# Performance work log

Measured on AMD Instinct MI355X. Metric: run time of the kernel, lower is better.

The kernel has to match this reference:

```python
import jax, jax.numpy as jnp
import numpy as np

B, PAD_LEN, HID, NB, NY = 1024, 127, 512, 128, 8
IN_DIM = 5 * (PAD_LEN + 1)          # LSTMCell input_size = 5*(pad_len+1)
MAX_TRIP, MAX_ROW = 10, 8
BARGE_PAR_WIDTH = 10.0


def setup_inputs() -> dict:
    key = jax.random.key(0)
    ks = jax.random.split(key, 12)
    s = 1.0 / np.sqrt(HID).astype(np.float32)
    return {
        "x": jax.random.normal(ks[0], (B, IN_DIM), jnp.float32),
        "h0": jnp.zeros((B, HID), jnp.float32),
        "c0": jnp.zeros((B, HID), jnp.float32),
        "W_ih": jax.random.normal(ks[1], (4 * HID, IN_DIM), jnp.float32) * s,
        "W_hh": jax.random.normal(ks[2], (4 * HID, HID), jnp.float32) * s,
        "b_ih": jax.random.normal(ks[3], (4 * HID,), jnp.float32) * s,
        "b_hh": jax.random.normal(ks[4], (4 * HID,), jnp.float32) * s,
        "W_fc": jax.random.normal(ks[5], (NB * NY, HID), jnp.float32) * s,
        "b_fc": jax.random.normal(ks[6], (NB * NY,), jnp.float32) * s,
        "block_size": jax.random.uniform(ks[7], (B, NB, 5), jnp.float32),
        "block_lengths_on_barge": jax.random.uniform(ks[8], (B, NY, MAX_TRIP, MAX_ROW), jnp.float32),
        "block_width_on_barge": jax.random.uniform(ks[9], (B, NY, MAX_TRIP, MAX_ROW), jnp.float32),
        "encoder_mask": jax.random.bernoulli(ks[10], 0.5, (B, NB, NY, PAD_LEN)),
        "block_mask": jnp.zeros((B, NB), bool),
        "barge_count": jax.random.randint(ks[11], (B, NY), 0, MAX_TRIP, jnp.int32),
        "barge_slot": -jnp.ones((B, NY, MAX_TRIP, MAX_ROW, 2), jnp.int32),
    }


def reference(x, h0, c0, W_ih, W_hh, b_ih, b_hh, W_fc, b_fc,
              block_size, block_lengths_on_barge, block_width_on_barge,
              encoder_mask, block_mask, barge_count, barge_slot):
    # ---- LSTMCell step (torch gate order: i, f, g, o) ----
    gates = x @ W_ih.T + b_ih + h0 @ W_hh.T + b_hh          # (B, 4H)
    i, f, g, o = jnp.split(gates, 4, axis=-1)
    c = jax.nn.sigmoid(f) * c0 + jax.nn.sigmoid(i) * jnp.tanh(g)
    h = jax.nn.sigmoid(o) * jnp.tanh(c)

    # ---- fc + masked softmax over (block, yard) joint actions ----
    logits = h @ W_fc.T + b_fc                               # (B, NB*NY)
    yard_feasible = jnp.any(encoder_mask, axis=-1)           # (B, NB, NY): block fits in some slot of yard
    valid = yard_feasible & (~block_mask)[:, :, None]        # unselected blocks only
    neg = jnp.asarray(-1e9, logits.dtype)
    probs = jax.nn.softmax(jnp.where(valid.reshape(valid.shape[0], -1), logits, neg), axis=-1)

    # ---- action decode + per-sample barge-slot scatter allocation ----
    Bsz = x.shape[0]
    bidx = jnp.arange(Bsz)
    action = jnp.argmax(probs, axis=-1)                      # greedy selection
    block_sel = action // NY
    yard_sel = (action % NY).astype(barge_count.dtype)
    cur = barge_count[bidx, yard_sel]                        # (B,) current barge idx per sample
    blen = block_size[bidx, block_sel, 0]                    # (B,)
    bwid = block_size[bidx, block_sel, 1]                    # (B,)

    widths = block_width_on_barge[bidx, yard_sel, cur]       # (B, MAX_ROW) gathered rows
    lens = block_lengths_on_barge[bidx, yard_sel, cur]       # (B, MAX_ROW)
    par_ok = widths <= BARGE_PAR_WIDTH                       # parallel-space feasibility per slot
    cand = jnp.where(par_ok, lens, -1.0)                     # invalid slots -> -1 (as in source)
    slot = jnp.argmax(cand, axis=-1)                         # best existing-length parallel slot

    barge_slot_new = barge_slot.at[bidx, yard_sel, cur, slot, 1].set(block_sel.astype(barge_slot.dtype))
    widths_new = block_width_on_barge.at[bidx, yard_sel, cur, slot].add(bwid)
    lengths_new = block_lengths_on_barge.at[bidx, yard_sel, cur, slot].max(blen)
    return probs, barge_slot_new, lengths_new, widths_new
```

## Files before the change

### kernel.cpp

```cpp
#include <hip/hip_runtime.h>
#include <math.h>

#define Bsz 1024
#define PADL 127
#define HID 512
#define NBb 128
#define NYd 8
#define INDIM 640
#define MTRIP 10
#define MROW 8
#define NBNY 1024
#define FOURH 2048

__device__ __forceinline__ float sigf(float x){ return 1.0f/(1.0f+expf(-x)); }

template<int TM>
__global__ __launch_bounds__(256) void gemm_bias(
    const float* __restrict__ A1, const float* __restrict__ B1, int K1,
    const float* __restrict__ A2, const float* __restrict__ B2, int K2,
    const float* __restrict__ bias1, const float* __restrict__ bias2,
    float* __restrict__ C, int ldc)
{
    constexpr int BM = TM*16;
    __shared__ float As[2][16][BM+4];
    __shared__ float Bs[2][16][68];
    const int tid = threadIdx.x;
    const int m0 = blockIdx.y*BM, n0 = blockIdx.x*64;

    const int ar = (TM==8) ? (tid>>1) : (tid>>2);
    const int ac = (TM==8) ? ((tid&1)*8) : ((tid&3)*4);
    const int br = tid>>2, bc = (tid&3)*4;

    const int tm = (tid>>4)*TM, tn = (tid&15)*4;

    float acc[TM][4];
    #pragma unroll
    for (int i=0;i<TM;i++){
        #pragma unroll
        for (int j=0;j<4;j++) acc[i][j]=0.f;
    }

    const int P1 = K1/16;
    const int nsteps = P1 + K2/16;

    float4 pa0, pa1, pb0;
    auto prefetch = [&](int s){
        const float* A; const float* B; int K; int k0;
        if (s < P1){ A=A1; B=B1; K=K1; k0 = s*16; }
        else       { A=A2; B=B2; K=K2; k0 = (s-P1)*16; }
        const float* ap = A + (size_t)(m0+ar)*K + k0 + ac;
        pa0 = *(const float4*)ap;
        if (TM==8) pa1 = *(const float4*)(ap+4);
        pb0 = *(const float4*)(B + (size_t)(n0+br)*K + k0 + bc);
    };
    auto stage = [&](int buf){
        As[buf][ac+0][ar]=pa0.x; As[buf][ac+1][ar]=pa0.y;
        As[buf][ac+2][ar]=pa0.z; As[buf][ac+3][ar]=pa0.w;
        if (TM==8){
            As[buf][ac+4][ar]=pa1.x; As[buf][ac+5][ar]=pa1.y;
            As[buf][ac+6][ar]=pa1.z; As[buf][ac+7][ar]=pa1.w;
        }
        Bs[buf][bc+0][br]=pb0.x; Bs[buf][bc+1][br]=pb0.y;
        Bs[buf][bc+2][br]=pb0.z; Bs[buf][bc+3][br]=pb0.w;
    };

    prefetch(0);
    stage(0);
    __syncthreads();
    int buf = 0;
    for (int s=0; s<nsteps; ++s){
        if (s+1 < nsteps) prefetch(s+1);
        #pragma unroll
        for (int kk=0; kk<16; ++kk){
            float a[TM], b[4];
            #pragma unroll
            for (int i=0;i<TM;i++) a[i] = As[buf][kk][tm+i];
            #pragma unroll
            for (int j=0;j<4;j++)  b[j] = Bs[buf][kk][tn+j];
            #pragma unroll
            for (int i=0;i<TM;i++)
                #pragma unroll
                for (int j=0;j<4;j++) acc[i][j] += a[i]*b[j];
        }
        if (s+1 < nsteps){
            stage(buf^1);
            __syncthreads();
            buf ^= 1;
        }
    }

    #pragma unroll
    for (int i=0;i<TM;i++){
        int row = m0+tm+i;
        #pragma unroll
        for (int j=0;j<4;j++){
            int col = n0+tn+j;
            float bsum = bias1[col] + (bias2 ? bias2[col] : 0.f);
            C[(size_t)row*ldc + col] = acc[i][j] + bsum;
        }
    }
}

__global__ __launch_bounds__(256) void lstm_kernel(const float* __restrict__ gates,
    const float* __restrict__ c0, float* __restrict__ h)
{
    int idx = blockIdx.x*256 + threadIdx.x;
    int b = idx >> 7, j4 = (idx & 127)*4;
    const float* g = gates + (size_t)b*FOURH;
    float4 iv = *(const float4*)(g + j4);
    float4 fv = *(const float4*)(g + 512 + j4);
    float4 gv = *(const float4*)(g + 1024 + j4);
    float4 ov = *(const float4*)(g + 1536 + j4);
    float4 cv = *(const float4*)(c0 + (size_t)b*HID + j4);
    float4 hv;
    hv.x = sigf(ov.x)*tanhf(sigf(fv.x)*cv.x + sigf(iv.x)*tanhf(gv.x));
    hv.y = sigf(ov.y)*tanhf(sigf(fv.y)*cv.y + sigf(iv.y)*tanhf(gv.y));
    hv.z = sigf(ov.z)*tanhf(sigf(fv.z)*cv.z + sigf(iv.z)*tanhf(gv.z));
    hv.w = sigf(ov.w)*tanhf(sigf(fv.w)*cv.w + sigf(iv.w)*tanhf(gv.w));
    *(float4*)(h + (size_t)b*HID + j4) = hv;
}

__device__ __forceinline__ int row_any(const int* __restrict__ p){
    #pragma unroll 1
    for (int j=0; j<124; j+=4){
        if (p[j] | p[j+1] | p[j+2] | p[j+3]) return 1;
    }
    return (p[124] | p[125] | p[126]) ? 1 : 0;
}

__global__ __launch_bounds__(256) void softmax_fused(
    const float* __restrict__ logits, const int* __restrict__ em,
    const int* __restrict__ bmask, const int* __restrict__ bcount,
    const float* __restrict__ bsize, const float* __restrict__ bwid_in,
    const float* __restrict__ blen_in,
    float* __restrict__ probs,
    int* __restrict__ pslot, int* __restrict__ pblock,
    float* __restrict__ pblen, float* __restrict__ pbwid)
{
    int b = blockIdx.x, t = threadIdx.x;
    __shared__ float red[256];
    __shared__ int  redi[256];
    const float* lrow = logits + (size_t)b*NBNY;

    float ml[4]; float mymax = -INFINITY;
    #pragma unroll
    for (int r=0;r<4;++r){
        int c = t + r*256;
        int nb = c >> 3;
        int v = 0;
        if (bmask[b*NBb + nb] == 0)
            v = row_any(em + (size_t)(b*NBNY + c)*PADL);
        float m = v ? lrow[c] : -1e9f;
        ml[r] = m; mymax = fmaxf(mymax, m);
    }
    red[t]=mymax; __syncthreads();
    for (int s=128;s>0;s>>=1){ if(t<s) red[t]=fmaxf(red[t],red[t+s]); __syncthreads(); }
    float rowmax = red[0]; __syncthreads();

    float p[4]; float mysum=0.f;
    #pragma unroll
    for (int r=0;r<4;++r){ p[r]=expf(ml[r]-rowmax); mysum+=p[r]; }
    red[t]=mysum; __syncthreads();
    for (int s=128;s>0;s>>=1){ if(t<s) red[t]+=red[t+s]; __syncthreads(); }
    float inv = 1.0f/red[0]; __syncthreads();

    float bv=-INFINITY; int bi=0;
    #pragma unroll
    for (int r=0;r<4;++r){
        int c = t + r*256;
        float pr = p[r]*inv;
        probs[(size_t)b*NBNY + c] = pr;
        if (pr > bv){ bv=pr; bi=c; }
    }
    red[t]=bv; redi[t]=bi; __syncthreads();
    for (int s=128;s>0;s>>=1){
        if (t<s){
            float ov=red[t+s]; int oi=redi[t+s];
            if (ov>red[t] || (ov==red[t] && oi<redi[t])){ red[t]=ov; redi[t]=oi; }
        }
        __syncthreads();
    }

    if (t==0){
        int a = redi[0];
        int blk = a / NYd, yard = a % NYd;
        int cur = bcount[b*NYd + yard];
        int base = ((b*NYd + yard)*MTRIP + cur)*MROW;
        float bestv = -INFINITY; int bests = 0;
        #pragma unroll
        for (int s=0;s<MROW;++s){
            float w = bwid_in[base+s];
            float l = blen_in[base+s];
            float cand = (w <= 10.0f) ? l : -1.0f;
            if (cand > bestv){ bestv=cand; bests=s; }
        }
        pslot[b]  = base + bests;
        pblock[b] = blk;
        pblen[b]  = bsize[(b*NBb + blk)*5 + 0];
        pbwid[b]  = bsize[(b*NBb + blk)*5 + 1];
    }
}

__global__ __launch_bounds__(256) void finalize_kernel(const int* __restrict__ bslot,
    const float* __restrict__ blen_in, const float* __restrict__ bwid_in,
    const int* __restrict__ pslot, const int* __restrict__ pblock,
    const float* __restrict__ pblen, const float* __restrict__ pbwid,
    float* __restrict__ out_slot, float* __restrict__ out_len, float* __restrict__ out_wid)
{
    int i = blockIdx.x*256 + threadIdx.x;
    if (i < Bsz*NYd*MTRIP*MROW*2){
        int b = i / (NYd*MTRIP*MROW*2);
        float v = (float)bslot[i];
        if (i == pslot[b]*2 + 1) v = (float)pblock[b];
        out_slot[i] = v;
    }
    if (i < Bsz*NYd*MTRIP*MROW){
        int b = i / (NYd*MTRIP*MROW);
        float l = blen_in[i], w = bwid_in[i];
        if (i == pslot[b]){ l = fmaxf(l, pblen[b]); w = w + pbwid[b]; }
        out_len[i] = l;
        out_wid[i] = w;
    }
}

extern "C" void kernel_launch(void* const* d_in, const int* in_sizes, int n_in,
                              void* d_out, int out_size, void* d_ws, size_t ws_size,
                              hipStream_t stream)
{
    const float* x    = (const float*)d_in[0];
    const float* h0   = (const float*)d_in[1];
    const float* c0   = (const float*)d_in[2];
    const float* Wih  = (const float*)d_in[3];
    const float* Whh  = (const float*)d_in[4];
    const float* bih  = (const float*)d_in[5];
    const float* bhh  = (const float*)d_in[6];
    const float* Wfc  = (const float*)d_in[7];
    const float* bfc  = (const float*)d_in[8];
    const float* bsize= (const float*)d_in[9];
    const float* blen = (const float*)d_in[10];
    const float* bwid = (const float*)d_in[11];
    const int*   em   = (const int*)d_in[12];
    const int*   bmask= (const int*)d_in[13];
    const int*   bcount=(const int*)d_in[14];
    const int*   bslot= (const int*)d_in[15];

    float* out      = (float*)d_out;
    float* probs    = out;
    float* out_slot = out + 1048576;
    float* out_len  = out + 1048576 + 1310720;
    float* out_wid  = out_len + 655360;

    float* ws     = (float*)d_ws;
    float* gates  = ws;
    float* h      = ws + 2097152;
    float* logits = ws + 2621440;
    int*   pslot  = (int*)(ws + 3670016);
    int*   pblock = (int*)(ws + 3671040);
    float* pblen  = ws + 3672064;
    float* pbwid  = ws + 3673088;

    gemm_bias<8><<<dim3(FOURH/64, Bsz/128), 256, 0, stream>>>(
        x, Wih, INDIM, h0, Whh, HID, bih, bhh, gates, FOURH);
    lstm_kernel<<<512, 256, 0, stream>>>(gates, c0, h);
    gemm_bias<4><<<dim3(NBNY/64, Bsz/64), 256, 0, stream>>>(
        h, Wfc, HID, nullptr, nullptr, 0, bfc, nullptr, logits, NBNY);
    softmax_fused<<<Bsz, 256, 0, stream>>>(logits, em, bmask, bcount, bsize, bwid, blen,
                                           probs, pslot, pblock, pblen, pbwid);
    finalize_kernel<<<5120, 256, 0, stream>>>(bslot, blen, bwid, pslot, pblock, pblen, pbwid,
                                              out_slot, out_len, out_wid);
}
```

Before: 810.0 us.

## Run gates GEMM on bf16x3 split-precision MFMA with concatenated K operands

Splits x|h0 and W_ih|W_hh into high and low bf16 parts, concatenated along K (1152), in two conversion kernels. The gates GEMM then runs on 16x16x32 bf16 MFMA using three products (hh, hl, lh) to approximate fp32 accuracy. The fc GEMM becomes a dedicated fp32 kernel with vectorized LDS reads. This trades scalar FP32 FMA work for matrix-core throughput, at the cost of extra conversion passes over the weights every call and a small precision loss.

```diff
diff --git a/kernel.cpp b/kernel.cpp
--- a/kernel.cpp
+++ b/kernel.cpp
@@ -11,92 +11,181 @@
 #define MROW 8
 #define NBNY 1024
 #define FOURH 2048
+#define KCAT 1152
+
+typedef short  bf16x8 __attribute__((ext_vector_type(8)));
+typedef float  f32x4  __attribute__((ext_vector_type(4)));
+typedef unsigned short u16x8 __attribute__((ext_vector_type(8)));
 
 __device__ __forceinline__ float sigf(float x){ return 1.0f/(1.0f+expf(-x)); }
 
-template<int TM>
-__global__ __launch_bounds__(256) void gemm_bias(
-    const float* __restrict__ A1, const float* __restrict__ B1, int K1,
-    const float* __restrict__ A2, const float* __restrict__ B2, int K2,
-    const float* __restrict__ bias1, const float* __restrict__ bias2,
-    float* __restrict__ C, int ldc)
-{
-    constexpr int BM = TM*16;
-    __shared__ float As[2][16][BM+4];
+__device__ __forceinline__ unsigned short bf16rn(float x){
+    unsigned int u = __float_as_uint(x);
+    unsigned int r = (u + 0x7FFFu + ((u>>16)&1u)) >> 16;
+    return (unsigned short)r;
+}
+
+__global__ __launch_bounds__(256) void convert_concat(
+    const float* __restrict__ src1, const float* __restrict__ src2,
+    unsigned short* __restrict__ dstH, unsigned short* __restrict__ dstL)
+{
+    int t = blockIdx.x*256 + threadIdx.x;
+    int r  = t / 144;
+    int c8 = t - r*144;
+    const float* p = (c8 < 80) ? (src1 + (size_t)r*INDIM + c8*8)
+                               : (src2 + (size_t)r*HID + (c8-80)*8);
+    float4 v0 = *(const float4*)p;
+    float4 v1 = *(const float4*)(p+4);
+    float v[8] = {v0.x,v0.y,v0.z,v0.w,v1.x,v1.y,v1.z,v1.w};
+    u16x8 hv, lv;
+    #pragma unroll
+    for (int i=0;i<8;++i){
+        unsigned short h = bf16rn(v[i]);
+        float hf = __uint_as_float(((unsigned int)h)<<16);
+        unsigned short l = bf16rn(v[i]-hf);
+        hv[i] = h; lv[i] = l;
+    }
+    size_t base = (size_t)r*KCAT + c8*8;
+    *(u16x8*)(dstH + base) = hv;
+    *(u16x8*)(dstL + base) = lv;
+}
+
+__global__ __launch_bounds__(256) void gemm_gates_mfma(
+    const unsigned short* __restrict__ Ah_g, const unsigned short* __restrict__ Al_g,
+    const unsigned short* __restrict__ Bh_g, const unsigned short* __restrict__ Bl_g,
+    const float* __restrict__ bih, const float* __restrict__ bhh,
+    float* __restrict__ gates)
+{
+    __shared__ __align__(16) unsigned short Ah_s[128*32];
+    __shared__ __align__(16) unsigned short Al_s[128*32];
+    __shared__ __align__(16) unsigned short Bh_s[64*32];
+    __shared__ __align__(16) unsigned short Bl_s[64*32];
+
+    const int t = threadIdx.x;
+    const int lane = t & 63;
+    const int w = t >> 6;
+    const int wr = w >> 1, wc = w & 1;
+    const int m0 = blockIdx.y*128, n0 = blockIdx.x*64;
+
+    const int fa0 = t*8;
+    const int fa1 = (256+t)*8;
+    const int fb  = t*8;
+    const int ar0 = fa0>>5, ac0 = fa0&31;
+    const int ar1 = fa1>>5, ac1 = fa1&31;
+    const int brow = fb>>5, bcol = fb&31;
+
+    f32x4 acc[4][2];
+    #pragma unroll
+    for (int m=0;m<4;++m){
+        #pragma unroll
+        for (int n=0;n<2;++n) acc[m][n] = (f32x4){0.f,0.f,0.f,0.f};
+    }
+
+    uint4 rah0, rah1, ral0, ral1, rbh, rbl;
+    auto load6 = [&](int k0){
+        rah0 = *(const uint4*)(Ah_g + (size_t)(m0+ar0)*KCAT + k0 + ac0);
+        rah1 = *(const uint4*)(Ah_g + (size_t)(m0+ar1)*KCAT + k0 + ac1);
+        ral0 = *(const uint4*)(Al_g + (size_t)(m0+ar0)*KCAT + k0 + ac0);
+        ral1 = *(const uint4*)(Al_g + (size_t)(m0+ar1)*KCAT + k0 + ac1);
+        rbh  = *(const uint4*)(Bh_g + (size_t)(n0+brow)*KCAT + k0 + bcol);
+        rbl  = *(const uint4*)(Bl_g + (size_t)(n0+brow)*KCAT + k0 + bcol);
+    };
+
+    load6(0);
+    for (int s=0; s<KCAT/32; ++s){
+        __syncthreads();
+        *(uint4*)&Ah_s[fa0] = rah0;  *(uint4*)&Ah_s[fa1] = rah1;
+        *(uint4*)&Al_s[fa0] = ral0;  *(uint4*)&Al_s[fa1] = ral1;
+        *(uint4*)&Bh_s[fb]  = rbh;   *(uint4*)&Bl_s[fb]  = rbl;
+        __syncthreads();
+        if (s+1 < KCAT/32) load6((s+1)*32);
+
+        const int kc = (lane>>4)*8;
+        bf16x8 afh[4], afl[4], bfh[2], bfl[2];
+        #pragma unroll
+        for (int m=0;m<4;++m){
+            int idx = (wr*64 + m*16 + (lane&15))*32 + kc;
+            afh[m] = *(const bf16x8*)&Ah_s[idx];
+            afl[m] = *(const bf16x8*)&Al_s[idx];
+        }
+        #pragma unroll
+        for (int n=0;n<2;++n){
+            int idx = (wc*32 + n*16 + (lane&15))*32 + kc;
+            bfh[n] = *(const bf16x8*)&Bh_s[idx];
+            bfl[n] = *(const bf16x8*)&Bl_s[idx];
+        }
+        #pragma unroll
+        for (int m=0;m<4;++m){
+            #pragma unroll
+            for (int n=0;n<2;++n){
+                acc[m][n] = __builtin_amdgcn_mfma_f32_16x16x32_bf16(afh[m], bfh[n], acc[m][n], 0,0,0);
+                acc[m][n] = __builtin_amdgcn_mfma_f32_16x16x32_bf16(afh[m], bfl[n], acc[m][n], 0,0,0);
+                acc[m][n] = __builtin_amdgcn_mfma_f32_16x16x32_bf16(afl[m], bfh[n], acc[m][n], 0,0,0);
+            }
+        }
+    }
+
+    #pragma unroll
+    for (int m=0;m<4;++m){
+        #pragma unroll
+        for (int n=0;n<2;++n){
+            int row = m0 + wr*64 + m*16 + ((lane>>4)<<2);
+            int col = n0 + wc*32 + n*16 + (lane&15);
+            float bsum = bih[col] + bhh[col];
+            #pragma unroll
+            for (int q=0;q<4;++q)
+                gates[(size_t)(row+q)*FOURH + col] = acc[m][n][q] + bsum;
+        }
+    }
+}
+
+__global__ __launch_bounds__(256) void gemm_fc_f32(
+    const float* __restrict__ A, const float* __restrict__ B,
+    const float* __restrict__ bias, float* __restrict__ C)
+{
+    __shared__ float As[2][16][68];
     __shared__ float Bs[2][16][68];
     const int tid = threadIdx.x;
-    const int m0 = blockIdx.y*BM, n0 = blockIdx.x*64;
-
-    const int ar = (TM==8) ? (tid>>1) : (tid>>2);
-    const int ac = (TM==8) ? ((tid&1)*8) : ((tid&3)*4);
-    const int br = tid>>2, bc = (tid&3)*4;
-
-    const int tm = (tid>>4)*TM, tn = (tid&15)*4;
-
-    float acc[TM][4];
-    #pragma unroll
-    for (int i=0;i<TM;i++){
-        #pragma unroll
-        for (int j=0;j<4;j++) acc[i][j]=0.f;
-    }
-
-    const int P1 = K1/16;
-    const int nsteps = P1 + K2/16;
-
-    float4 pa0, pa1, pb0;
-    auto prefetch = [&](int s){
-        const float* A; const float* B; int K; int k0;
-        if (s < P1){ A=A1; B=B1; K=K1; k0 = s*16; }
-        else       { A=A2; B=B2; K=K2; k0 = (s-P1)*16; }
-        const float* ap = A + (size_t)(m0+ar)*K + k0 + ac;
-        pa0 = *(const float4*)ap;
-        if (TM==8) pa1 = *(const float4*)(ap+4);
-        pb0 = *(const float4*)(B + (size_t)(n0+br)*K + k0 + bc);
+    const int m0 = blockIdx.y*64, n0 = blockIdx.x*64;
+    const int lr = tid>>2, lc = (tid&3)*4;
+    const int tm = (tid>>4)*4, tn = (tid&15)*4;
+    float acc[4][4] = {{0,0,0,0},{0,0,0,0},{0,0,0,0},{0,0,0,0}};
+
+    float4 pa, pb;
+    auto prefetch = [&](int k0){
+        pa = *(const float4*)(A + (size_t)(m0+lr)*HID + k0 + lc);
+        pb = *(const float4*)(B + (size_t)(n0+lr)*HID + k0 + lc);
     };
     auto stage = [&](int buf){
-        As[buf][ac+0][ar]=pa0.x; As[buf][ac+1][ar]=pa0.y;
-        As[buf][ac+2][ar]=pa0.z; As[buf][ac+3][ar]=pa0.w;
-        if (TM==8){
-            As[buf][ac+4][ar]=pa1.x; As[buf][ac+5][ar]=pa1.y;
-            As[buf][ac+6][ar]=pa1.z; As[buf][ac+7][ar]=pa1.w;
-        }
-        Bs[buf][bc+0][br]=pb0.x; Bs[buf][bc+1][br]=pb0.y;
-        Bs[buf][bc+2][br]=pb0.z; Bs[buf][bc+3][br]=pb0.w;
+        As[buf][lc+0][lr]=pa.x; As[buf][lc+1][lr]=pa.y;
+        As[buf][lc+2][lr]=pa.z; As[buf][lc+3][lr]=pa.w;
+        Bs[buf][lc+0][lr]=pb.x; Bs[buf][lc+1][lr]=pb.y;
+        Bs[buf][lc+2][lr]=pb.z; Bs[buf][lc+3][lr]=pb.w;
     };
 
-    prefetch(0);
-    stage(0);
-    __syncthreads();
+    prefetch(0); stage(0); __syncthreads();
     int buf = 0;
-    for (int s=0; s<nsteps; ++s){
-        if (s+1 < nsteps) prefetch(s+1);
+    for (int s=0; s<HID/16; ++s){
+        if (s+1 < HID/16) prefetch((s+1)*16);
         #pragma unroll
         for (int kk=0; kk<16; ++kk){
-            float a[TM], b[4];
+            float4 a = *(const float4*)&As[buf][kk][tm];
+            float4 b = *(const float4*)&Bs[buf][kk][tn];
+            float a4[4]={a.x,a.y,a.z,a.w}, b4[4]={b.x,b.y,b.z,b.w};
             #pragma unroll
-            for (int i=0;i<TM;i++) a[i] = As[buf][kk][tm+i];
-            #pragma unroll
-            for (int j=0;j<4;j++)  b[j] = Bs[buf][kk][tn+j];
-            #pragma unroll
-            for (int i=0;i<TM;i++)
+            for (int i=0;i<4;i++)
                 #pragma unroll
-                for (int j=0;j<4;j++) acc[i][j] += a[i]*b[j];
-        }
-        if (s+1 < nsteps){
-            stage(buf^1);
-            __syncthreads();
-            buf ^= 1;
-        }
-    }
-
-    #pragma unroll
-    for (int i=0;i<TM;i++){
+                for (int j=0;j<4;j++) acc[i][j] += a4[i]*b4[j];
+        }
+        if (s+1 < HID/16){ stage(buf^1); __syncthreads(); buf ^= 1; }
+    }
+    #pragma unroll
+    for (int i=0;i<4;i++){
         int row = m0+tm+i;
         #pragma unroll
         for (int j=0;j<4;j++){
             int col = n0+tn+j;
-            float bsum = bias1[col] + (bias2 ? bias2[col] : 0.f);
-            C[(size_t)row*ldc + col] = acc[i][j] + bsum;
+            C[(size_t)row*NBNY + col] = acc[i][j] + bias[col];
         }
     }
 }
@@ -254,16 +343,21 @@
     float* gates  = ws;
     float* h      = ws + 2097152;
     float* logits = ws + 2621440;
-    int*   pslot  = (int*)(ws + 3670016);
-    int*   pblock = (int*)(ws + 3671040);
-    float* pblen  = ws + 3672064;
-    float* pbwid  = ws + 3673088;
-
-    gemm_bias<8><<<dim3(FOURH/64, Bsz/128), 256, 0, stream>>>(
-        x, Wih, INDIM, h0, Whh, HID, bih, bhh, gates, FOURH);
+    unsigned short* Ah = (unsigned short*)(ws + 3670016);
+    unsigned short* Al = (unsigned short*)(ws + 4259840);
+    unsigned short* Bh = (unsigned short*)(ws + 4849664);
+    unsigned short* Bl = (unsigned short*)(ws + 6029312);
+    int*   pslot  = (int*)(ws + 7208960);
+    int*   pblock = (int*)(ws + 7209984);
+    float* pblen  = ws + 7211008;
+    float* pbwid  = ws + 7212032;
+
+    convert_concat<<<576, 256, 0, stream>>>(x, h0, Ah, Al);
+    convert_concat<<<1152, 256, 0, stream>>>(Wih, Whh, Bh, Bl);
+    gemm_gates_mfma<<<dim3(FOURH/64, Bsz/128), 256, 0, stream>>>(
+        Ah, Al, Bh, Bl, bih, bhh, gates);
     lstm_kernel<<<512, 256, 0, stream>>>(gates, c0, h);
-    gemm_bias<4><<<dim3(NBNY/64, Bsz/64), 256, 0, stream>>>(
-        h, Wfc, HID, nullptr, nullptr, 0, bfc, nullptr, logits, NBNY);
+    gemm_fc_f32<<<dim3(NBNY/64, Bsz/64), 256, 0, stream>>>(h, Wfc, bfc, logits);
     softmax_fused<<<Bsz, 256, 0, stream>>>(logits, em, bmask, bcount, bsize, bwid, blen,
                                            probs, pslot, pblock, pblen, pbwid);
     finalize_kernel<<<5120, 256, 0, stream>>>(bslot, blen, bwid, pslot, pblock, pblen, pbwid,
```

Result: faster. 730.9 us (-9.8%).
